# Kernel tuning notes

Measured on AMD Instinct MI355X. Metric: run time of the kernel, lower is better.

The kernel has to match this reference:

```python
import jax, jax.numpy as jnp
import numpy as np

B, T, C, H, NIN = 4, 16384, 512, 8, 2
D = C // H


def setup_inputs() -> dict:
    key = jax.random.key(0)
    ks = jax.random.split(key, 12)
    s = 1.0 / np.sqrt(C)
    return {
        "x1": jax.random.normal(ks[0], (B, T, C), jnp.float32),
        "x2": jax.random.normal(ks[1], (B, T, C), jnp.float32),
        "y0": jax.random.normal(ks[2], (B, T, C), jnp.float32),
        "y1": jax.random.normal(ks[3], (B, T, C), jnp.float32),
        "Wq": jax.random.normal(ks[4], (C, C), jnp.float32) * s,
        "bq": jnp.zeros((C,), jnp.float32),
        "Wk": jax.random.normal(ks[5], (C, C), jnp.float32) * s,
        "bk": jnp.zeros((C,), jnp.float32),
        "Wv": jax.random.normal(ks[6], (NIN, C, C), jnp.float32) * s,
        "bv": jnp.zeros((NIN, C), jnp.float32),
        "Wp": jax.random.normal(ks[7], (C, C), jnp.float32) * s,
        "bp": jnp.zeros((C,), jnp.float32),
    }


def _heads(x):
    # [B, T, C] -> [B, H, T, D]
    b, t, c = x.shape
    return x.reshape(b, t, H, D).transpose(0, 2, 1, 3)


def reference(x1, x2, y0, y1, Wq, bq, Wk, bk, Wv, bv, Wp, bp):
    # q, k: softmax feature maps over head dim
    q = jax.nn.softmax(_heads(x1 @ Wq + bq), axis=-1)  # [B,H,T1,D]
    k = jax.nn.softmax(_heads(x2 @ Wk + bk), axis=-1)  # [B,H,T2,D]
    # v = sum of per-input value projections
    ys = jnp.stack([y0, y1], axis=0)  # [NIN,B,T2,C]
    v = jnp.einsum('ibtc,icd->btd', ys, Wv) + bv.sum(axis=0)
    v = _heads(v)  # [B,H,T2,D]
    # linear attention: k^T v then q @ (kv)
    k_v = jnp.einsum('bhtd,bhte->bhde', k, v)      # [B,H,D,D]
    q_k_v = jnp.einsum('bhsd,bhde->bhse', q, k_v)  # [B,H,T1,D]
    k_cumsum = k.sum(axis=-2, keepdims=True)       # [B,H,1,D]
    D_inv = 1.0 / (q * k_cumsum).sum(axis=-1, keepdims=True)
    out = q_k_v * D_inv                            # [B,H,T1,D]
    out = out.transpose(0, 2, 1, 3).reshape(x1.shape[0], x1.shape[1], C)
    return out @ Wp + bp
```

## Files before the change

kernel.cpp:

```cpp
#include <hip/hip_runtime.h>
#include <cstdint>
#include <cstddef>

#define BB 4
#define TT 16384
#define CC 512
#define HH 8
#define DD 64
#define MTOT (BB*TT)

typedef __attribute__((ext_vector_type(4))) float f32x4;
typedef __bf16 bf16;
typedef __attribute__((ext_vector_type(8))) bf16 bf16x8;
typedef __attribute__((ext_vector_type(4))) bf16 bf16x4;

static __device__ __forceinline__ float b2f(bf16 x) { return (float)x; }
static __device__ __forceinline__ bf16  f2b(float x) { return (bf16)x; }

static __device__ __forceinline__ void gload16(const bf16* src, bf16* ldsbase) {
    __builtin_amdgcn_global_load_lds(
        (const __attribute__((address_space(1))) void*)src,
        (__attribute__((address_space(3))) void*)ldsbase, 16, 0, 0);
}

__global__ __launch_bounds__(256) void transpose_w5(
    const float* __restrict__ W0, const float* __restrict__ W1,
    const float* __restrict__ W2, const float* __restrict__ W3,
    const float* __restrict__ W4,
    bf16* __restrict__ T0, bf16* __restrict__ T1, bf16* __restrict__ T2,
    bf16* __restrict__ T3, bf16* __restrict__ T4)
{
    __shared__ float tile[32][33];
    const int which = blockIdx.x >> 8;
    const float* W = which == 0 ? W0 : which == 1 ? W1 : which == 2 ? W2
                   : which == 3 ? W3 : W4;
    bf16* Wt = which == 0 ? T0 : which == 1 ? T1 : which == 2 ? T2
             : which == 3 ? T3 : T4;
    const int t = blockIdx.x & 255;
    const int r0 = (t >> 4) * 32, c0 = (t & 15) * 32;
    const int tid = threadIdx.x;
    {
        int r = tid >> 3, c4 = (tid & 7) << 2;
        float4 v = *(const float4*)(W + (size_t)(r0 + r) * 512 + c0 + c4);
        tile[r][c4 + 0] = v.x; tile[r][c4 + 1] = v.y;
        tile[r][c4 + 2] = v.z; tile[r][c4 + 3] = v.w;
    }
    __syncthreads();
    {
        int n = tid >> 3, k4 = (tid & 7) << 2;
        bf16x4 o;
        o[0] = f2b(tile[k4 + 0][n]); o[1] = f2b(tile[k4 + 1][n]);
        o[2] = f2b(tile[k4 + 2][n]); o[3] = f2b(tile[k4 + 3][n]);
        *(bf16x4*)(Wt + (size_t)(c0 + n) * 512 + r0 + k4) = o;
    }
}

template<int MODE>
__global__ __launch_bounds__(512) void gemm_proj(
    const float* A0, const float* A1, const bf16* Abf,
    const bf16* Wt0, const bf16* Wt1,
    const float* bias0, const float* bias1,
    bf16* outb, float* outf, int m_base)
{
    __shared__ bf16 Asm[128 * 40];
    __shared__ bf16 Bsm[2][512 * 32];

    const int tid = threadIdx.x;
    const int lane = tid & 63;
    const int w = tid >> 6;
    const int l15 = lane & 15, lg = lane >> 4;
    const int lq = lane >> 2, lc = lane & 3;
    const size_t m0 = (size_t)(blockIdx.x + m_base) * 128;

    f32x4 acc[8][4];
#pragma unroll
    for (int m = 0; m < 8; ++m)
#pragma unroll
        for (int n = 0; n < 4; ++n) acc[m][n] = (f32x4){0.f, 0.f, 0.f, 0.f};

    const int KSTEPS = (MODE == 2) ? 32 : 16;

    const int arow_f = tid >> 2, acol_f = (tid & 3) << 2;
    const int arow_b = tid >> 2, acol_b = (tid & 3) << 3;

    float4 apf0, apf1;
    bf16x8 apfb;

    auto issueA = [&](int t) {
        if (MODE == 3) {
            apfb = *(const bf16x8*)(Abf + (m0 + arow_b) * CC + (t & 15) * 32 + acol_b);
        } else {
            const float* Af = (MODE == 2 && t >= 16) ? A1 : A0;
            apf0 = *(const float4*)(Af + (m0 + arow_f) * CC + (t & 15) * 32 + acol_f);
            apf1 = *(const float4*)(Af + (m0 + arow_f) * CC + (t & 15) * 32 + acol_f + 16);
        }
    };
    auto writeA = [&]() {
        if (MODE == 3) {
            *(bf16x8*)&Asm[arow_b * 40 + acol_b] = apfb;
        } else {
            bf16x4 s0, s1;
            s0[0] = f2b(apf0.x); s0[1] = f2b(apf0.y);
            s0[2] = f2b(apf0.z); s0[3] = f2b(apf0.w);
            s1[0] = f2b(apf1.x); s1[1] = f2b(apf1.y);
            s1[2] = f2b(apf1.z); s1[3] = f2b(apf1.w);
            *(bf16x4*)&Asm[arow_f * 40 + acol_f] = s0;
            *(bf16x4*)&Asm[arow_f * 40 + acol_f + 16] = s1;
        }
    };
    auto issueB = [&](int t, int buf) {
        const bf16* Wt = (MODE == 2 && t >= 16) ? Wt1 : Wt0;
#pragma unroll
        for (int r = 0; r < 4; ++r) {
            int rowbase = r * 128 + w * 16;
            gload16(Wt + (size_t)(rowbase + lq) * CC + (t & 15) * 32 + lc * 8,
                    &Bsm[buf][rowbase * 32]);
        }
    };

    issueA(0);
    issueB(0, 0);
    writeA();
    asm volatile("s_waitcnt lgkmcnt(0)" ::: "memory");

    int cur = 0;
    for (int ko = 0; ko < KSTEPS; ++ko) {
        const bool more = ko + 1 < KSTEPS;
        if (more) { issueA(ko + 1); issueB(ko + 1, cur ^ 1); }
        if (more) {
            if (MODE == 3) asm volatile("s_waitcnt vmcnt(5)" ::: "memory");
            else           asm volatile("s_waitcnt vmcnt(6)" ::: "memory");
        } else {
            asm volatile("s_waitcnt vmcnt(0)" ::: "memory");
        }
        __builtin_amdgcn_s_barrier();
        bf16x8 af[8], bfv[4];
#pragma unroll
        for (int m = 0; m < 8; ++m)
            af[m] = *(const bf16x8*)&Asm[(m * 16 + l15) * 40 + lg * 8];
#pragma unroll
        for (int n = 0; n < 4; ++n)
            bfv[n] = *(const bf16x8*)&Bsm[cur][(w * 64 + n * 16 + l15) * 32 + lg * 8];
#pragma unroll
        for (int m = 0; m < 8; ++m)
#pragma unroll
            for (int n = 0; n < 4; ++n)
                acc[m][n] = __builtin_amdgcn_mfma_f32_16x16x32_bf16(
                    af[m], bfv[n], acc[m][n], 0, 0, 0);
        __builtin_amdgcn_s_barrier();
        if (more) {
            writeA();
            asm volatile("s_waitcnt lgkmcnt(0)" ::: "memory");
        }
        cur ^= 1;
    }

    float bias[4];
#pragma unroll
    for (int n = 0; n < 4; ++n) {
        int col = w * 64 + n * 16 + l15;
        float bvv = bias0 ? bias0[col] : 0.f;
        if (MODE == 2) bvv += bias1[col];
        bias[n] = bvv;
    }
#pragma unroll
    for (int m = 0; m < 8; ++m) {
#pragma unroll
        for (int reg = 0; reg < 4; ++reg) {
            int r = m * 16 + lg * 4 + reg;
            float v0 = acc[m][0][reg] + bias[0];
            float v1 = acc[m][1][reg] + bias[1];
            float v2 = acc[m][2][reg] + bias[2];
            float v3 = acc[m][3][reg] + bias[3];
            if (MODE == 0) {
                float mx = fmaxf(fmaxf(v0, v1), fmaxf(v2, v3));
#pragma unroll
                for (int s = 1; s < 16; s <<= 1) mx = fmaxf(mx, __shfl_xor(mx, s, 64));
                v0 = __expf(v0 - mx); v1 = __expf(v1 - mx);
                v2 = __expf(v2 - mx); v3 = __expf(v3 - mx);
                float sm = v0 + v1 + v2 + v3;
#pragma unroll
                for (int s = 1; s < 16; s <<= 1) sm += __shfl_xor(sm, s, 64);
                float inv = 1.0f / sm;
                v0 *= inv; v1 *= inv; v2 *= inv; v3 *= inv;
            }
            size_t rowoff = (m0 + r) * CC + w * 64 + l15;
            if (MODE == 3) {
                outf[rowoff + 0]  = v0; outf[rowoff + 16] = v1;
                outf[rowoff + 32] = v2; outf[rowoff + 48] = v3;
            } else {
                outb[rowoff + 0]  = f2b(v0); outb[rowoff + 16] = f2b(v1);
                outb[rowoff + 32] = f2b(v2); outb[rowoff + 48] = f2b(v3);
            }
        }
    }
}

__global__ __launch_bounds__(256) void kv_partial2(
    const bf16* __restrict__ Kb, const bf16* __restrict__ Vb,
    float* __restrict__ part)
{
    __shared__ float Ks[32][68], Vs[32][68];
    const int tid = threadIdx.x;
    const int bh = blockIdx.x >> 5, chunk = blockIdx.x & 31;
    const int b = bh >> 3, h = bh & 7;
    const size_t base = (size_t)b * TT * CC + h * 64;
    const int d0 = (tid & 15) * 4, e0 = (tid >> 4) * 4;

    float acc[4][4];
#pragma unroll
    for (int i = 0; i < 4; ++i)
#pragma unroll
        for (int j = 0; j < 4; ++j) acc[i][j] = 0.f;
    float ks[4] = {0.f, 0.f, 0.f, 0.f};

    const int tstart = chunk * 512;
    for (int t0 = tstart; t0 < tstart + 512; t0 += 32) {
        __syncthreads();
#pragma unroll
        for (int rep = 0; rep < 2; ++rep) {
            int idx = (tid + rep * 256) * 4;
            int t = idx >> 6, dc = idx & 63;
            const bf16* gk = Kb + base + (size_t)(t0 + t) * CC + dc;
            const bf16* gv = Vb + base + (size_t)(t0 + t) * CC + dc;
            bf16x4 k4 = *(const bf16x4*)gk;
            bf16x4 v4 = *(const bf16x4*)gv;
            *(float4*)&Ks[t][dc] = make_float4(b2f(k4[0]), b2f(k4[1]), b2f(k4[2]), b2f(k4[3]));
            *(float4*)&Vs[t][dc] = make_float4(b2f(v4[0]), b2f(v4[1]), b2f(v4[2]), b2f(v4[3]));
        }
        __syncthreads();
#pragma unroll 8
        for (int tt = 0; tt < 32; ++tt) {
            float kf[4], vf[4];
#pragma unroll
            for (int i = 0; i < 4; ++i) { kf[i] = Ks[tt][d0 + i]; vf[i] = Vs[tt][e0 + i]; }
            if (e0 == 0) {
#pragma unroll
                for (int i = 0; i < 4; ++i) ks[i] += kf[i];
            }
#pragma unroll
            for (int i = 0; i < 4; ++i)
#pragma unroll
                for (int j = 0; j < 4; ++j) acc[i][j] += kf[i] * vf[j];
        }
    }

    float* p = part + (size_t)blockIdx.x * 4160;
#pragma unroll
    for (int i = 0; i < 4; ++i)
#pragma unroll
        for (int j = 0; j < 4; ++j) p[(d0 + i) * 64 + (e0 + j)] = acc[i][j];
    if (tid < 16) {
#pragma unroll
        for (int i = 0; i < 4; ++i) p[4096 + d0 + i] = ks[i];
    }
}

__global__ __launch_bounds__(256) void kv_reduce(
    const float* __restrict__ part, float* __restrict__ kvT,
    float* __restrict__ ksum)
{
    const int bh = blockIdx.x >> 3, sl = blockIdx.x & 7;
    const int tid = threadIdx.x;
    const float* p0 = part + (size_t)bh * 32 * 4160;
    const int i0 = sl * 520, i1 = i0 + 520;
    for (int i = i0 + tid; i < i1; i += 256) {
        float s = 0.f;
        for (int c = 0; c < 32; ++c) s += p0[(size_t)c * 4160 + i];
        if (i < 4096) {
            int d = i >> 6, e = i & 63;
            kvT[(size_t)bh * 4096 + e * 64 + d] = s;
        } else {
            ksum[bh * 64 + (i - 4096)] = s;
        }
    }
}

__global__ __launch_bounds__(256) void qkv_norm2(
    bf16* Qb, const float* __restrict__ kvT, const float* __restrict__ ksum)
{
    __shared__ float Qs[64][68];
    __shared__ float KVs[64][68];
    __shared__ float ksm[8][64];
    const int tid = threadIdx.x;
    const size_t t0 = (size_t)blockIdx.x * 64;
    const int b = (int)(t0 / TT);
    const int rg = tid >> 4, cg = tid & 15;

    for (int i = tid; i < 512; i += 256) ksm[i >> 6][i & 63] = ksum[b * 512 + i];

    for (int h = 0; h < 8; ++h) {
        __syncthreads();
        const float* kvb = kvT + (size_t)(b * 8 + h) * 4096;
#pragma unroll
        for (int rep = 0; rep < 4; ++rep) {
            int idx = (tid + rep * 256) * 4;
            int rr = idx >> 6, dc = idx & 63;
            bf16x4 q4 = *(const bf16x4*)(Qb + (t0 + rr) * CC + h * 64 + dc);
            *(float4*)&Qs[rr][dc] = make_float4(b2f(q4[0]), b2f(q4[1]), b2f(q4[2]), b2f(q4[3]));
            float4 v4 = *(const float4*)(kvb + rr * 64 + dc);
            KVs[dc + 0][rr] = v4.x; KVs[dc + 1][rr] = v4.y;
            KVs[dc + 2][rr] = v4.z; KVs[dc + 3][rr] = v4.w;
        }
        __syncthreads();

        float acc[4][4];
#pragma unroll
        for (int i = 0; i < 4; ++i)
#pragma unroll
            for (int j = 0; j < 4; ++j) acc[i][j] = 0.f;
        float dot[4] = {0.f, 0.f, 0.f, 0.f};

        for (int d = 0; d < 64; ++d) {
            float ksd = ksm[h][d];
            float4 kv4 = *(const float4*)&KVs[d][cg * 4];
            float q[4];
#pragma unroll
            for (int i = 0; i < 4; ++i) {
                q[i] = Qs[rg * 4 + i][d];
                dot[i] += q[i] * ksd;
            }
#pragma unroll
            for (int i = 0; i < 4; ++i) {
                acc[i][0] += q[i] * kv4.x; acc[i][1] += q[i] * kv4.y;
                acc[i][2] += q[i] * kv4.z; acc[i][3] += q[i] * kv4.w;
            }
        }
#pragma unroll
        for (int i = 0; i < 4; ++i) {
            float dinv = 1.0f / dot[i];
            bf16x4 o;
#pragma unroll
            for (int j = 0; j < 4; ++j) o[j] = f2b(acc[i][j] * dinv);
            *(bf16x4*)(Qb + (t0 + rg * 4 + i) * CC + h * 64 + cg * 4) = o;
        }
    }
}

extern "C" void kernel_launch(void* const* d_in, const int* in_sizes, int n_in,
                              void* d_out, int out_size, void* d_ws, size_t ws_size,
                              hipStream_t stream)
{
    const float* x1 = (const float*)d_in[0];
    const float* x2 = (const float*)d_in[1];
    const float* y0 = (const float*)d_in[2];
    const float* y1 = (const float*)d_in[3];
    const float* Wq = (const float*)d_in[4];
    const float* bq = (const float*)d_in[5];
    const float* Wk = (const float*)d_in[6];
    const float* bk = (const float*)d_in[7];
    const float* Wv = (const float*)d_in[8];
    const float* bv = (const float*)d_in[9];
    const float* Wp = (const float*)d_in[10];
    const float* bp = (const float*)d_in[11];
    (void)in_sizes; (void)n_in; (void)out_size;

    char* ws = (char*)d_ws;
    size_t off = 0;
    auto alloc = [&](size_t bytes) -> void* {
        void* p = ws + off;
        off += (bytes + 255) & ~(size_t)255;
        return p;
    };
    bf16* WtQ  = (bf16*)alloc((size_t)512 * 512 * 2);
    bf16* WtK  = (bf16*)alloc((size_t)512 * 512 * 2);
    bf16* WtV0 = (bf16*)alloc((size_t)512 * 512 * 2);
    bf16* WtV1 = (bf16*)alloc((size_t)512 * 512 * 2);
    bf16* WtP  = (bf16*)alloc((size_t)512 * 512 * 2);
    float* ksum = (float*)alloc((size_t)32 * 64 * 4);
    float* kvT  = (float*)alloc((size_t)32 * 4096 * 4);
    float* part = (float*)alloc((size_t)1024 * 4160 * 4);
    bf16* Acopy = (bf16*)alloc((size_t)16 * 128 * CC * 2);

    const size_t QBYTES = (size_t)MTOT * CC * 2;
    bf16* Qb_ws = nullptr;
    if (ws_size >= off + QBYTES + 256) Qb_ws = (bf16*)alloc(QBYTES);

    bf16* Kb = (bf16*)d_out;
    bf16* Vb = Kb + (size_t)MTOT * CC;
    float* outF = (float*)d_out;

    transpose_w5<<<1280, 256, 0, stream>>>(Wq, Wk, Wv, Wv + (size_t)512 * 512, Wp,
                                           WtQ, WtK, WtV0, WtV1, WtP);

    gemm_proj<0><<<MTOT / 128, 512, 0, stream>>>(x2, nullptr, nullptr, WtK, nullptr,
                                                 bk, nullptr, Kb, nullptr, 0);
    gemm_proj<2><<<MTOT / 128, 512, 0, stream>>>(y0, y1, nullptr, WtV0, WtV1,
                                                 bv, bv + 512, Vb, nullptr, 0);
    kv_partial2<<<1024, 256, 0, stream>>>(Kb, Vb, part);
    kv_reduce<<<256, 256, 0, stream>>>(part, kvT, ksum);

    if (Qb_ws) {
        gemm_proj<0><<<MTOT / 128, 512, 0, stream>>>(x1, nullptr, nullptr, WtQ, nullptr,
                                                     bq, nullptr, Qb_ws, nullptr, 0);
        qkv_norm2<<<1024, 256, 0, stream>>>(Qb_ws, kvT, ksum);
        gemm_proj<3><<<MTOT / 128, 512, 0, stream>>>(nullptr, nullptr, (const bf16*)Qb_ws,
                                                     WtP, nullptr, bp, nullptr,
                                                     nullptr, outF, 0);
    } else {
        bf16* Qb = Kb;
        gemm_proj<0><<<MTOT / 128, 512, 0, stream>>>(x1, nullptr, nullptr, WtQ, nullptr,
                                                     bq, nullptr, Qb, nullptr, 0);
        qkv_norm2<<<1024, 256, 0, stream>>>(Qb, kvT, ksum);
        hipMemcpyAsync(Acopy, Qb, (size_t)16 * 128 * CC * 2, hipMemcpyDeviceToDevice,
                       stream);
        const int starts[5] = {256, 128, 64, 32, 16};
        const int counts[5] = {256, 128, 64, 32, 16};
        for (int p = 0; p < 5; ++p) {
            gemm_proj<3><<<counts[p], 512, 0, stream>>>(nullptr, nullptr, (const bf16*)Qb,
                                                        WtP, nullptr, bp, nullptr,
                                                        nullptr, outF, starts[p]);
        }
        gemm_proj<3><<<16, 512, 0, stream>>>(nullptr, nullptr, (const bf16*)Acopy,
                                             WtP, nullptr, bp, nullptr,
                                             nullptr, outF, 0);
    }
}
```

Baseline: 526.6 us.

## Double GEMM K-tile to 64 with XOR-swizzled B LDS layout

The projection GEMM now consumes 64 K-elements per step instead of 32, halving the number of barrier-separated iterations and doubling the loads in flight per step. The B tile in LDS is stored with an XOR swizzle on 8-element chunks to avoid bank conflicts on the wider rows, and the A tile padding changes to 72. This raises LDS use (about 146 KB) and register pressure for the doubled fragments, which may limit occupancy.

```diff
diff --git a/kernel.cpp b/kernel.cpp
--- a/kernel.cpp
+++ b/kernel.cpp
@@ -62,59 +62,65 @@
     const float* bias0, const float* bias1,
     bf16* outb, float* outf, int m_base)
 {
-    __shared__ bf16 Asm[128 * 40];
-    __shared__ bf16 Bsm[2][512 * 32];
+    constexpr int KSTEPS = (MODE == 2) ? 16 : 8;
+    __shared__ bf16 Asm[128 * 72];
+    __shared__ bf16 Bsm[2][512 * 64];
 
     const int tid = threadIdx.x;
     const int lane = tid & 63;
     const int w = tid >> 6;
     const int l15 = lane & 15, lg = lane >> 4;
-    const int lq = lane >> 2, lc = lane & 3;
     const size_t m0 = (size_t)(blockIdx.x + m_base) * 128;
 
+    const int arow = tid >> 2, ac16 = (tid & 3) << 4;
+    const int blr = lane >> 3;
+    const int bsc = ((lane & 7) ^ blr) << 3;
+
     f32x4 acc[8][4];
 #pragma unroll
     for (int m = 0; m < 8; ++m)
 #pragma unroll
         for (int n = 0; n < 4; ++n) acc[m][n] = (f32x4){0.f, 0.f, 0.f, 0.f};
 
-    const int KSTEPS = (MODE == 2) ? 32 : 16;
-
-    const int arow_f = tid >> 2, acol_f = (tid & 3) << 2;
-    const int arow_b = tid >> 2, acol_b = (tid & 3) << 3;
-
-    float4 apf0, apf1;
-    bf16x8 apfb;
+    float4 apf[4];
+    bf16x8 apb[2];
 
     auto issueA = [&](int t) {
         if (MODE == 3) {
-            apfb = *(const bf16x8*)(Abf + (m0 + arow_b) * CC + (t & 15) * 32 + acol_b);
+#pragma unroll
+            for (int j = 0; j < 2; ++j)
+                apb[j] = *(const bf16x8*)(Abf + (m0 + arow) * CC + (t & 7) * 64
+                                          + ac16 + j * 8);
         } else {
-            const float* Af = (MODE == 2 && t >= 16) ? A1 : A0;
-            apf0 = *(const float4*)(Af + (m0 + arow_f) * CC + (t & 15) * 32 + acol_f);
-            apf1 = *(const float4*)(Af + (m0 + arow_f) * CC + (t & 15) * 32 + acol_f + 16);
+            const float* Af = (MODE == 2 && t >= 8) ? A1 : A0;
+#pragma unroll
+            for (int j = 0; j < 4; ++j)
+                apf[j] = *(const float4*)(Af + (m0 + arow) * CC + (t & 7) * 64
+                                          + ac16 + j * 4);
         }
     };
     auto writeA = [&]() {
         if (MODE == 3) {
-            *(bf16x8*)&Asm[arow_b * 40 + acol_b] = apfb;
+#pragma unroll
+            for (int j = 0; j < 2; ++j)
+                *(bf16x8*)&Asm[arow * 72 + ac16 + j * 8] = apb[j];
         } else {
-            bf16x4 s0, s1;
-            s0[0] = f2b(apf0.x); s0[1] = f2b(apf0.y);
-            s0[2] = f2b(apf0.z); s0[3] = f2b(apf0.w);
-            s1[0] = f2b(apf1.x); s1[1] = f2b(apf1.y);
-            s1[2] = f2b(apf1.z); s1[3] = f2b(apf1.w);
-            *(bf16x4*)&Asm[arow_f * 40 + acol_f] = s0;
-            *(bf16x4*)&Asm[arow_f * 40 + acol_f + 16] = s1;
+#pragma unroll
+            for (int j = 0; j < 4; ++j) {
+                bf16x4 s;
+                s[0] = f2b(apf[j].x); s[1] = f2b(apf[j].y);
+                s[2] = f2b(apf[j].z); s[3] = f2b(apf[j].w);
+                *(bf16x4*)&Asm[arow * 72 + ac16 + j * 4] = s;
+            }
         }
     };
     auto issueB = [&](int t, int buf) {
-        const bf16* Wt = (MODE == 2 && t >= 16) ? Wt1 : Wt0;
-#pragma unroll
-        for (int r = 0; r < 4; ++r) {
-            int rowbase = r * 128 + w * 16;
-            gload16(Wt + (size_t)(rowbase + lq) * CC + (t & 15) * 32 + lc * 8,
-                    &Bsm[buf][rowbase * 32]);
+        const bf16* Wt = (MODE == 2 && t >= 8) ? Wt1 : Wt0;
+#pragma unroll
+        for (int g = 0; g < 8; ++g) {
+            int rowbase = w * 64 + g * 8;
+            gload16(Wt + (size_t)(rowbase + blr) * CC + (t & 7) * 64 + bsc,
+                    &Bsm[buf][rowbase * 64]);
         }
     };
 
@@ -128,25 +134,35 @@
         const bool more = ko + 1 < KSTEPS;
         if (more) { issueA(ko + 1); issueB(ko + 1, cur ^ 1); }
         if (more) {
-            if (MODE == 3) asm volatile("s_waitcnt vmcnt(5)" ::: "memory");
-            else           asm volatile("s_waitcnt vmcnt(6)" ::: "memory");
+            if (MODE == 3) asm volatile("s_waitcnt vmcnt(10)" ::: "memory");
+            else           asm volatile("s_waitcnt vmcnt(12)" ::: "memory");
         } else {
             asm volatile("s_waitcnt vmcnt(0)" ::: "memory");
         }
         __builtin_amdgcn_s_barrier();
-        bf16x8 af[8], bfv[4];
+        bf16x8 af[8][2], bfv[4][2];
 #pragma unroll
         for (int m = 0; m < 8; ++m)
-            af[m] = *(const bf16x8*)&Asm[(m * 16 + l15) * 40 + lg * 8];
-#pragma unroll
-        for (int n = 0; n < 4; ++n)
-            bfv[n] = *(const bf16x8*)&Bsm[cur][(w * 64 + n * 16 + l15) * 32 + lg * 8];
-#pragma unroll
-        for (int m = 0; m < 8; ++m)
-#pragma unroll
-            for (int n = 0; n < 4; ++n)
-                acc[m][n] = __builtin_amdgcn_mfma_f32_16x16x32_bf16(
-                    af[m], bfv[n], acc[m][n], 0, 0, 0);
+#pragma unroll
+            for (int kk = 0; kk < 2; ++kk)
+                af[m][kk] = *(const bf16x8*)&Asm[(m * 16 + l15) * 72 + kk * 32 + lg * 8];
+#pragma unroll
+        for (int n = 0; n < 4; ++n) {
+            int row = w * 64 + n * 16 + l15;
+            int swz = (l15 & 7) << 3;
+#pragma unroll
+            for (int kk = 0; kk < 2; ++kk)
+                bfv[n][kk] = *(const bf16x8*)&Bsm[cur][row * 64
+                                                      + ((kk * 32 + lg * 8) ^ swz)];
+        }
+#pragma unroll
+        for (int kk = 0; kk < 2; ++kk)
+#pragma unroll
+            for (int m = 0; m < 8; ++m)
+#pragma unroll
+                for (int n = 0; n < 4; ++n)
+                    acc[m][n] = __builtin_amdgcn_mfma_f32_16x16x32_bf16(
+                        af[m][kk], bfv[n][kk], acc[m][n], 0, 0, 0);
         __builtin_amdgcn_s_barrier();
         if (more) {
             writeA();
```

After: 491.5 us. 1.07x faster.
